# Optimization experiments

Hardware: AMD Instinct MI355X
Metric: run time of the kernel (lower is better)

The kernel has to match this reference:

```python
import jax, jax.numpy as jnp
import numpy as np

V, I, H, OUT = 50000, 512, 1024, 2   # node_size, input_dim, hidden_dim, out_dim
P, L = 256, 64                       # num paths, max path length
NH = 32                              # num attention heads
HD = H // NH


def setup_inputs() -> dict:
    key = jax.random.key(0)
    ks = jax.random.split(key, 10)
    paths = jax.random.randint(ks[0], (P, L), 0, V)          # padded path token ids
    lengths = jax.random.randint(ks[1], (P,), 1, L + 1)       # true path lengths in [1, L]
    g = lambda k, shape, s: jax.random.normal(k, shape, jnp.float32) * s
    return {
        "paths": paths,
        "lengths": lengths,
        "emb_table": g(ks[2], (V, I), 0.1),
        "W_ih": g(ks[3], (4 * H, I), 0.02),
        "W_hh": g(ks[4], (4 * H, H), 0.02),
        "b_ih": jnp.zeros((4 * H,), jnp.float32),
        "b_hh": jnp.zeros((4 * H,), jnp.float32),
        "W_in": g(ks[5], (3 * H, H), 0.02),   # packed q,k,v in_proj (torch layout)
        "b_in": jnp.zeros((3 * H,), jnp.float32),
        "W_out": g(ks[6], (H, H), 0.02),
        "b_out": jnp.zeros((H,), jnp.float32),
        "W_lin": g(ks[7], (OUT, H), 0.02),
        "b_lin": jnp.zeros((OUT,), jnp.float32),
    }


def reference(paths, lengths, emb_table, W_ih, W_hh, b_ih, b_hh,
              W_in, b_in, W_out, b_out, W_lin, b_lin):
    p = paths.shape[0]
    x = emb_table[paths]                 # [P, L, I] (batched embedding of all ragged paths)
    xs = jnp.swapaxes(x, 0, 1)           # [L, P, I] time-major for scan
    b = b_ih + b_hh

    def step(carry, xt):                 # single-layer LSTM, torch gate order i,f,g,o
        h, c = carry
        gates = xt @ W_ih.T + h @ W_hh.T + b          # [P, 4H]
        i_g, f_g, g_g, o_g = jnp.split(gates, 4, axis=-1)
        c = jax.nn.sigmoid(f_g) * c + jax.nn.sigmoid(i_g) * jnp.tanh(g_g)
        h = jax.nn.sigmoid(o_g) * jnp.tanh(c)
        return (h, c), h

    h0 = jnp.zeros((p, H), x.dtype)
    _, hs = jax.lax.scan(step, (h0, h0), xs)          # [L, P, H]
    # final hidden of each path at its true length (equiv. to per-path h_n in the torch loop)
    final_h = hs[lengths - 1, jnp.arange(p)]          # [P, H]
    sum_hidden = final_h[None]                        # [1, P, H]  (seq=1, batch=P)

    # nn.MultiheadAttention(sum_hidden, sum_hidden, sum_hidden), seq_len = 1
    qkv = sum_hidden @ W_in.T + b_in                  # [1, P, 3H]
    q, k, v = jnp.split(qkv, 3, axis=-1)
    qh = q.reshape(1, p, NH, HD)
    kh = k.reshape(1, p, NH, HD)
    vh = v.reshape(1, p, NH, HD)
    scale = 1.0 / np.sqrt(HD).astype(np.float32)
    scores = jnp.einsum('qpnd,kpnd->pnqk', qh * scale, kh)   # [P, NH, 1, 1]
    attn = jax.nn.softmax(scores, axis=-1)
    ctx = jnp.einsum('pnqk,kpnd->qpnd', attn, vh).reshape(1, p, H)
    attn_out = ctx @ W_out.T + b_out                  # [1, P, H]

    # MaxPool2d((P,1)) on (C=1, H=P, W=hidden): max over the P paths
    pooled = jnp.max(attn_out, axis=1, keepdims=True)  # [1, 1, H]
    out = jax.nn.sigmoid(pooled @ W_lin.T + b_lin)     # [1, 1, OUT]
    return out
```

## Files before the change

kernel.cpp:

```cpp
#include <hip/hip_runtime.h>
#include <stdint.h>

typedef unsigned short u16;
typedef unsigned int u32;
typedef __attribute__((ext_vector_type(8))) short s16x8;
typedef __attribute__((ext_vector_type(4))) float f32x4;

#define P_ 256
#define L_ 64
#define IDIM 512
#define H_ 1024

__device__ __forceinline__ u16 f2bf(float f){union{float f;u32 u;}v;v.f=f;u32 u=v.u;return (u16)((u+0x7FFFu+((u>>16)&1u))>>16);}
__device__ __forceinline__ float sigf(float x){return 1.0f/(1.0f+__expf(-x));}
__device__ __forceinline__ float tanhf_(float x){return 1.0f-2.0f/(__expf(2.0f*x)+1.0f);}

__device__ __forceinline__ s16x8 pack8v(float4 a, float4 b){
  s16x8 r;
  r[0]=(short)f2bf(a.x); r[1]=(short)f2bf(a.y); r[2]=(short)f2bf(a.z); r[3]=(short)f2bf(a.w);
  r[4]=(short)f2bf(b.x); r[5]=(short)f2bf(b.y); r[6]=(short)f2bf(b.z); r[7]=(short)f2bf(b.w);
  return r;
}
__device__ __forceinline__ s16x8 pack8(const float* s){
  return pack8v(*(const float4*)s, *(const float4*)(s+4));
}
__device__ __forceinline__ void st16_coh(u16* addr, s16x8 v){
  asm volatile("global_store_dwordx4 %0, %1, off sc0 sc1" :: "v"(addr), "v"(v) : "memory");
}
__device__ __forceinline__ void st_pair(u16* addr, float hv, int lane){
  u32 b = (u32)f2bf(hv);
  u32 other = __shfl_xor(b, 1);
  if ((lane & 1) == 0) {
    u32 w = b | (other << 16);
    __hip_atomic_store((u32*)addr, w, __ATOMIC_RELAXED, __HIP_MEMORY_SCOPE_AGENT);
  }
}
__device__ __forceinline__ void poll_ctr(u32* ctr, u32 target, int wid, int lane){
  if (wid == 0 && lane == 0) {
    while (__hip_atomic_load(ctr, __ATOMIC_RELAXED, __HIP_MEMORY_SCOPE_AGENT) < target)
      __builtin_amdgcn_s_sleep(2);
  }
  asm volatile("" ::: "memory");
  __syncthreads();
}

__global__ void __launch_bounds__(256, 1)
tagger_net(const int* __restrict__ paths, const int* __restrict__ lengths,
           const float* __restrict__ emb,
           const float* __restrict__ Wih, const float* __restrict__ Whh,
           const float* __restrict__ bih, const float* __restrict__ bhh,
           const float* __restrict__ Win, const float* __restrict__ bin,
           const float* __restrict__ Wout, const float* __restrict__ bout,
           const float* __restrict__ Wlin, const float* __restrict__ blin,
           u16* __restrict__ X, u16* __restrict__ Hbuf,
           u16* __restrict__ vbuf, float* __restrict__ pmax,
           u32* ctrs, float* __restrict__ out)
{
  __shared__ __align__(16) float S[16384];
  const int tid  = threadIdx.x;
  const int wid  = tid >> 6, lane = tid & 63;
  const int lrow = lane & 15, lgrp = lane >> 4;
  const int bid  = blockIdx.x;
  const int g = bid >> 6, jb = bid & 63;
  const int p0 = g * 64, j0 = jb * 16;
  u32* ctr = ctrs + g * 64;

  for (int it = 0; it < 16; ++it) {
    int e = (it * 256 + tid) * 8;
    int row = e >> 9, col = e & 511;
    int tok = paths[(p0 + row) * L_ + jb];
    const float* s = emb + (size_t)tok * IDIM + col;
    float4 a = *(const float4*)s, b4 = *(const float4*)(s + 4);
    st16_coh(X + ((size_t)jb * P_ + p0 + row) * IDIM + col, pack8v(a, b4));
  }
#pragma unroll
  for (int i = 0; i < 2; ++i) {
    int idx = tid * 2 + i;
    int row = idx >> 3, cp = idx & 7;
    __hip_atomic_store((u32*)&Hbuf[(size_t)(p0 + row) * H_ + j0 + cp * 2], 0u,
                       __ATOMIC_RELAXED, __HIP_MEMORY_SCOPE_AGENT);
  }
  __syncthreads();
  if (tid == 0) __hip_atomic_fetch_add(ctr, 1u, __ATOMIC_RELAXED, __HIP_MEMORY_SCOPE_AGENT);

  s16x8 breg[12][4];
#pragma unroll
  for (int i = 0; i < 12; ++i) {
    const int k = (wid + 4 * i) * 32 + lgrp * 8;
#pragma unroll
    for (int fn = 0; fn < 4; ++fn) {
      const int n = fn * H_ + j0 + lrow;
      const float* src = (k < IDIM) ? (Wih + (size_t)n * IDIM + k)
                                    : (Whh + (size_t)n * H_ + (k - IDIM));
      breg[i][fn] = pack8(src);
    }
  }

  const int prow = p0 + wid * 16 + lgrp * 4;
  int lenr[4]; float biasv[4];
#pragma unroll
  for (int r2 = 0; r2 < 4; ++r2) lenr[r2] = lengths[prow + r2];
#pragma unroll
  for (int fn = 0; fn < 4; ++fn) {
    int n = fn * H_ + j0 + lrow;
    biasv[fn] = bih[n] + bhh[n];
  }
  float cst[4] = {0.f,0.f,0.f,0.f}, hst[4] = {0.f,0.f,0.f,0.f};

  poll_ctr(ctr, 64u, wid, lane);

  const size_t aX = (size_t)(p0 + lrow) * IDIM + lgrp * 8;
  const size_t aH = (size_t)(p0 + lrow) * H_   + lgrp * 8;

  s16x8 fx[4][4];
#define LOADX(T) do { \
    const u16* Xt_ = X + (size_t)(T) * (P_ * IDIM) + aX; \
    _Pragma("unroll") \
    for (int i_ = 0; i_ < 4; ++i_) { \
      const int k0_ = wid * 32 + i_ * 128; \
      _Pragma("unroll") \
      for (int fm_ = 0; fm_ < 4; ++fm_) \
        fx[i_][fm_] = *(const s16x8*)(Xt_ + (size_t)fm_ * (16 * IDIM) + k0_); \
    } } while (0)

  LOADX(0);

  for (int t = 0; t < L_; ++t) {
    const u16* Hr = Hbuf + (size_t)t * (P_ * H_);
    u16*       Hw = Hbuf + (size_t)(t + 1) * (P_ * H_);

    f32x4 acc[4][4];
#pragma unroll
    for (int a = 0; a < 4; ++a)
#pragma unroll
      for (int b = 0; b < 4; ++b)
#pragma unroll
        for (int e = 0; e < 4; ++e) acc[a][b][e] = 0.0f;

#pragma unroll
    for (int i = 0; i < 4; ++i)
#pragma unroll
      for (int fm = 0; fm < 4; ++fm)
#pragma unroll
        for (int fn = 0; fn < 4; ++fn)
          acc[fm][fn] = __builtin_amdgcn_mfma_f32_16x16x32_bf16(fx[i][fm], breg[i][fn], acc[fm][fn], 0, 0, 0);

    poll_ctr(ctr, 64u * (u32)(t + 1), wid, lane);

    const u16* Hp = Hr + aH;
#pragma unroll
    for (int half = 0; half < 2; ++half) {
      s16x8 fh[4][4];
#pragma unroll
      for (int i = 0; i < 4; ++i) {
        const int kh = wid * 32 + (half * 4 + i) * 128;
#pragma unroll
        for (int fm = 0; fm < 4; ++fm)
          fh[i][fm] = *(const s16x8*)(Hp + (size_t)fm * (16 * H_) + kh);
      }
#pragma unroll
      for (int i = 0; i < 4; ++i)
#pragma unroll
        for (int fm = 0; fm < 4; ++fm)
#pragma unroll
          for (int fn = 0; fn < 4; ++fn)
            acc[fm][fn] = __builtin_amdgcn_mfma_f32_16x16x32_bf16(fh[i][fm], breg[4 + half * 4 + i][fn], acc[fm][fn], 0, 0, 0);
    }

    const int tp1 = (t < L_ - 1) ? (t + 1) : (L_ - 1);
    LOADX(tp1);

#pragma unroll
    for (int fm = 0; fm < 4; ++fm)
#pragma unroll
      for (int fn = 0; fn < 4; ++fn)
        *(f32x4*)&S[((wid * 16) + fm * 4 + fn) * 256 + lane * 4] = acc[fm][fn];
    __syncthreads();
    f32x4 red[4];
#pragma unroll
    for (int fn = 0; fn < 4; ++fn) {
      red[fn] = *(const f32x4*)&S[(wid * 4 + fn) * 256 + lane * 4];
#pragma unroll
      for (int w = 1; w < 4; ++w)
        red[fn] += *(const f32x4*)&S[(w * 16 + wid * 4 + fn) * 256 + lane * 4];
    }

#pragma unroll
    for (int r2 = 0; r2 < 4; ++r2) {
      if (t < lenr[r2]) {
        float gi = red[0][r2] + biasv[0];
        float gf = red[1][r2] + biasv[1];
        float gg = red[2][r2] + biasv[2];
        float go = red[3][r2] + biasv[3];
        float cn = sigf(gf) * cst[r2] + sigf(gi) * tanhf_(gg);
        cst[r2] = cn;
        hst[r2] = sigf(go) * tanhf_(cn);
      }
      st_pair(&Hw[(size_t)(prow + r2) * H_ + j0 + lrow], hst[r2], lane);
    }
    __syncthreads();
    if (tid == 0) __hip_atomic_fetch_add(ctr, 1u, __ATOMIC_RELAXED, __HIP_MEMORY_SCOPE_AGENT);
  }

  const u16* hfin = Hbuf + (size_t)L_ * (P_ * H_);
  poll_ctr(ctr, 64u * 65u, wid, lane);

  {
    f32x4 acc2[4];
#pragma unroll
    for (int a = 0; a < 4; ++a)
#pragma unroll
      for (int e = 0; e < 4; ++e) acc2[a][e] = 0.0f;
    const u16* hp = hfin + aH;
    const float* wv = Win + (size_t)(2 * H_ + j0 + lrow) * H_;
#pragma unroll
    for (int ic = 0; ic < 8; ++ic) {
      const int k0 = wid * 256 + ic * 32;
      s16x8 fbv = pack8(wv + k0 + lgrp * 8);
#pragma unroll
      for (int fm = 0; fm < 4; ++fm) {
        s16x8 fav = *(const s16x8*)(hp + (size_t)fm * (16 * H_) + k0);
        acc2[fm] = __builtin_amdgcn_mfma_f32_16x16x32_bf16(fav, fbv, acc2[fm], 0, 0, 0);
      }
    }
#pragma unroll
    for (int fm = 0; fm < 4; ++fm)
      *(f32x4*)&S[(wid * 4 + fm) * 256 + lane * 4] = acc2[fm];
    __syncthreads();
    f32x4 rv = *(const f32x4*)&S[(wid) * 256 + lane * 4];
#pragma unroll
    for (int w = 1; w < 4; ++w)
      rv += *(const f32x4*)&S[(w * 4 + wid) * 256 + lane * 4];
    float bvj = bin[2 * H_ + j0 + lrow];
#pragma unroll
    for (int r2 = 0; r2 < 4; ++r2)
      st_pair(&vbuf[(size_t)(prow + r2) * H_ + j0 + lrow], rv[r2] + bvj, lane);
  }
  __syncthreads();
  if (tid == 0) __hip_atomic_fetch_add(ctr, 1u, __ATOMIC_RELAXED, __HIP_MEMORY_SCOPE_AGENT);
  poll_ctr(ctr, 64u * 66u, wid, lane);

  {
    f32x4 acc2[4];
#pragma unroll
    for (int a = 0; a < 4; ++a)
#pragma unroll
      for (int e = 0; e < 4; ++e) acc2[a][e] = 0.0f;
    const u16* vp = vbuf + aH;
    const float* wo = Wout + (size_t)(j0 + lrow) * H_;
#pragma unroll
    for (int ic = 0; ic < 8; ++ic) {
      const int k0 = wid * 256 + ic * 32;
      s16x8 fbv = pack8(wo + k0 + lgrp * 8);
#pragma unroll
      for (int fm = 0; fm < 4; ++fm) {
        s16x8 fav = *(const s16x8*)(vp + (size_t)fm * (16 * H_) + k0);
        acc2[fm] = __builtin_amdgcn_mfma_f32_16x16x32_bf16(fav, fbv, acc2[fm], 0, 0, 0);
      }
    }
#pragma unroll
    for (int fm = 0; fm < 4; ++fm)
      *(f32x4*)&S[(wid * 4 + fm) * 256 + lane * 4] = acc2[fm];
    __syncthreads();
    f32x4 rv = *(const f32x4*)&S[(wid) * 256 + lane * 4];
#pragma unroll
    for (int w = 1; w < 4; ++w)
      rv += *(const f32x4*)&S[(w * 4 + wid) * 256 + lane * 4];
    float bo = bout[j0 + lrow];
    float m = fmaxf(fmaxf(rv[0], rv[1]), fmaxf(rv[2], rv[3])) + bo;
    __syncthreads();
    S[(wid * 4 + lgrp) * 16 + lrow] = m;
    __syncthreads();
    if (tid < 16) {
      float mx = S[tid];
#pragma unroll
      for (int s2 = 1; s2 < 16; ++s2) mx = fmaxf(mx, S[s2 * 16 + tid]);
      __hip_atomic_store(&pmax[(size_t)g * H_ + j0 + tid], mx, __ATOMIC_RELAXED, __HIP_MEMORY_SCOPE_AGENT);
    }
  }
  __syncthreads();
  if (tid == 0) __hip_atomic_fetch_add(ctr, 1u, __ATOMIC_RELAXED, __HIP_MEMORY_SCOPE_AGENT);

  if (bid != 0) return;

  if (wid == 0 && lane == 0) {
    for (int g2 = 0; g2 < 4; ++g2)
      while (__hip_atomic_load(ctrs + g2 * 64, __ATOMIC_RELAXED, __HIP_MEMORY_SCOPE_AGENT) < 64u * 67u)
        __builtin_amdgcn_s_sleep(2);
  }
  asm volatile("" ::: "memory");
  __syncthreads();
  {
    int j4 = tid * 4;
    float s0 = 0.f, s1 = 0.f;
#pragma unroll
    for (int e = 0; e < 4; ++e) {
      float pv = pmax[j4 + e];
#pragma unroll
      for (int gg2 = 1; gg2 < 4; ++gg2) pv = fmaxf(pv, pmax[gg2 * H_ + j4 + e]);
      s0 += pv * Wlin[j4 + e];
      s1 += pv * Wlin[H_ + j4 + e];
    }
    S[tid] = s0; S[256 + tid] = s1;
    __syncthreads();
    for (int s2 = 128; s2 > 0; s2 >>= 1) {
      if (tid < s2) { S[tid] += S[tid + s2]; S[256 + tid] += S[256 + tid + s2]; }
      __syncthreads();
    }
    if (tid == 0) {
      out[0] = sigf(S[0] + blin[0]);
      out[1] = sigf(S[256] + blin[1]);
    }
  }
}

extern "C" void kernel_launch(void* const* d_in, const int* in_sizes, int n_in,
                              void* d_out, int out_size, void* d_ws, size_t ws_size,
                              hipStream_t stream) {
  const int*   paths   = (const int*)d_in[0];
  const int*   lengths = (const int*)d_in[1];
  const float* emb     = (const float*)d_in[2];
  const float* Wih     = (const float*)d_in[3];
  const float* Whh     = (const float*)d_in[4];
  const float* bih     = (const float*)d_in[5];
  const float* bhh     = (const float*)d_in[6];
  const float* Win     = (const float*)d_in[7];
  const float* bin     = (const float*)d_in[8];
  const float* Wout    = (const float*)d_in[9];
  const float* bout    = (const float*)d_in[10];
  const float* Wlin    = (const float*)d_in[11];
  const float* blin    = (const float*)d_in[12];
  float* out = (float*)d_out;

  char* ws = (char*)d_ws;
  u32*   ctrs   = (u32*)  (ws);
  float* pmax   = (float*)(ws + 4096);
  u16*   X      = (u16*)  (ws + 32768);
  u16*   Hbuf   = (u16*)  (ws + 16810240);
  u16*   vbuf   = (u16*)  (ws + 50888960);

  hipMemsetAsync(ctrs, 0, 1024, stream);
  tagger_net<<<256, 256, 0, stream>>>(paths, lengths, emb, Wih, Whh, bih, bhh,
                                      Win, bin, Wout, bout, Wlin, blin,
                                      X, Hbuf, vbuf, pmax, ctrs, out);
}
```

Before: 630.7 us.

## Split LSTM hidden columns across twice as many persistent blocks with just-in-time embedding gather

Doubles the grid from 256 to 512 blocks. Each block now owns 8 hidden units instead of 16, packing all four gates into two 16-wide MFMA N-tiles, and gates are recombined with a lane shuffle. The upfront embedding gather for all timesteps is replaced by gathering step t+2 inside the recurrence, and H loads are interleaved with MFMAs in smaller chunks. This halves per-block weight registers and per-step MFMA work to shorten the serial step latency. In exchange it doubles the blocks participating in each per-group counter barrier, and it requires two blocks per CU to be co-resident or the spin barrier deadlocks.

```diff
diff --git a/kernel.cpp b/kernel.cpp
--- a/kernel.cpp
+++ b/kernel.cpp
@@ -10,6 +10,7 @@
 #define L_ 64
 #define IDIM 512
 #define H_ 1024
+#define PH (P_ * H_)
 
 __device__ __forceinline__ u16 f2bf(float f){union{float f;u32 u;}v;v.f=f;u32 u=v.u;return (u16)((u+0x7FFFu+((u>>16)&1u))>>16);}
 __device__ __forceinline__ float sigf(float x){return 1.0f/(1.0f+__expf(-x));}
@@ -27,24 +28,16 @@
 __device__ __forceinline__ void st16_coh(u16* addr, s16x8 v){
   asm volatile("global_store_dwordx4 %0, %1, off sc0 sc1" :: "v"(addr), "v"(v) : "memory");
 }
-__device__ __forceinline__ void st_pair(u16* addr, float hv, int lane){
-  u32 b = (u32)f2bf(hv);
-  u32 other = __shfl_xor(b, 1);
-  if ((lane & 1) == 0) {
-    u32 w = b | (other << 16);
-    __hip_atomic_store((u32*)addr, w, __ATOMIC_RELAXED, __HIP_MEMORY_SCOPE_AGENT);
-  }
-}
 __device__ __forceinline__ void poll_ctr(u32* ctr, u32 target, int wid, int lane){
   if (wid == 0 && lane == 0) {
     while (__hip_atomic_load(ctr, __ATOMIC_RELAXED, __HIP_MEMORY_SCOPE_AGENT) < target)
-      __builtin_amdgcn_s_sleep(2);
+      __builtin_amdgcn_s_sleep(1);
   }
   asm volatile("" ::: "memory");
   __syncthreads();
 }
 
-__global__ void __launch_bounds__(256, 1)
+__global__ void __launch_bounds__(256, 2)
 tagger_net(const int* __restrict__ paths, const int* __restrict__ lengths,
            const float* __restrict__ emb,
            const float* __restrict__ Wih, const float* __restrict__ Whh,
@@ -56,40 +49,37 @@
            u16* __restrict__ vbuf, float* __restrict__ pmax,
            u32* ctrs, float* __restrict__ out)
 {
-  __shared__ __align__(16) float S[16384];
+  __shared__ __align__(16) float S[8192];
   const int tid  = threadIdx.x;
   const int wid  = tid >> 6, lane = tid & 63;
   const int lrow = lane & 15, lgrp = lane >> 4;
   const int bid  = blockIdx.x;
-  const int g = bid >> 6, jb = bid & 63;
-  const int p0 = g * 64, j0 = jb * 16;
+  const int g = bid >> 7, jb2 = bid & 127;
+  const int p0 = g * 64, j0 = jb2 * 8;
   u32* ctr = ctrs + g * 64;
 
-  for (int it = 0; it < 16; ++it) {
-    int e = (it * 256 + tid) * 8;
-    int row = e >> 9, col = e & 511;
-    int tok = paths[(p0 + row) * L_ + jb];
-    const float* s = emb + (size_t)tok * IDIM + col;
-    float4 a = *(const float4*)s, b4 = *(const float4*)(s + 4);
-    st16_coh(X + ((size_t)jb * P_ + p0 + row) * IDIM + col, pack8v(a, b4));
-  }
-#pragma unroll
-  for (int i = 0; i < 2; ++i) {
-    int idx = tid * 2 + i;
-    int row = idx >> 3, cp = idx & 7;
-    __hip_atomic_store((u32*)&Hbuf[(size_t)(p0 + row) * H_ + j0 + cp * 2], 0u,
+  if (wid == 0) {
+    int t0 = jb2 >> 6, row = jb2 & 63;
+    int tok = paths[(p0 + row) * L_ + t0];
+    const float* s = emb + (size_t)tok * IDIM + lane * 8;
+    st16_coh(X + ((size_t)t0 * P_ + p0 + row) * IDIM + lane * 8,
+             pack8v(*(const float4*)s, *(const float4*)(s + 4)));
+  }
+  {
+    int row = tid >> 2, cp = (tid & 3) * 2;
+    __hip_atomic_store((u32*)&Hbuf[(size_t)(p0 + row) * H_ + j0 + cp], 0u,
                        __ATOMIC_RELAXED, __HIP_MEMORY_SCOPE_AGENT);
   }
   __syncthreads();
   if (tid == 0) __hip_atomic_fetch_add(ctr, 1u, __ATOMIC_RELAXED, __HIP_MEMORY_SCOPE_AGENT);
 
-  s16x8 breg[12][4];
+  s16x8 breg[12][2];
 #pragma unroll
   for (int i = 0; i < 12; ++i) {
     const int k = (wid + 4 * i) * 32 + lgrp * 8;
 #pragma unroll
-    for (int fn = 0; fn < 4; ++fn) {
-      const int n = fn * H_ + j0 + lrow;
+    for (int fn = 0; fn < 2; ++fn) {
+      const int n = (fn * 2 + (lrow >> 3)) * H_ + j0 + (lrow & 7);
       const float* src = (k < IDIM) ? (Wih + (size_t)n * IDIM + k)
                                     : (Whh + (size_t)n * H_ + (k - IDIM));
       breg[i][fn] = pack8(src);
@@ -97,185 +87,204 @@
   }
 
   const int prow = p0 + wid * 16 + lgrp * 4;
-  int lenr[4]; float biasv[4];
-#pragma unroll
-  for (int r2 = 0; r2 < 4; ++r2) lenr[r2] = lengths[prow + r2];
-#pragma unroll
-  for (int fn = 0; fn < 4; ++fn) {
-    int n = fn * H_ + j0 + lrow;
-    biasv[fn] = bih[n] + bhh[n];
-  }
+  int lenr[4];
+#pragma unroll
+  for (int r = 0; r < 4; ++r) lenr[r] = lengths[prow + r];
+  const int ju = j0 + (lrow & 7);
+  const float bias_i = bih[ju] + bhh[ju];
+  const float bias_f = bih[H_ + ju] + bhh[H_ + ju];
+  const float bias_g = bih[2 * H_ + ju] + bhh[2 * H_ + ju];
+  const float bias_o = bih[3 * H_ + ju] + bhh[3 * H_ + ju];
   float cst[4] = {0.f,0.f,0.f,0.f}, hst[4] = {0.f,0.f,0.f,0.f};
-
-  poll_ctr(ctr, 64u, wid, lane);
 
   const size_t aX = (size_t)(p0 + lrow) * IDIM + lgrp * 8;
   const size_t aH = (size_t)(p0 + lrow) * H_   + lgrp * 8;
 
-  s16x8 fx[4][4];
-#define LOADX(T) do { \
+  poll_ctr(ctr, 128u, wid, lane);
+
+#define MM(FR, I0) do { \
+    _Pragma("unroll") \
+    for (int j_ = 0; j_ < 2; ++j_) \
+      _Pragma("unroll") \
+      for (int fm_ = 0; fm_ < 4; ++fm_) \
+        _Pragma("unroll") \
+        for (int fn_ = 0; fn_ < 2; ++fn_) \
+          acc[fm_][fn_] = __builtin_amdgcn_mfma_f32_16x16x32_bf16(FR[j_][fm_], breg[(I0)+j_][fn_], acc[fm_][fn_], 0, 0, 0); \
+  } while (0)
+
+#define LDX2(DST, T, C0) do { \
     const u16* Xt_ = X + (size_t)(T) * (P_ * IDIM) + aX; \
     _Pragma("unroll") \
-    for (int i_ = 0; i_ < 4; ++i_) { \
-      const int k0_ = wid * 32 + i_ * 128; \
+    for (int j_ = 0; j_ < 2; ++j_) { \
+      const int k0_ = (wid + 4 * ((C0) + j_)) * 32; \
       _Pragma("unroll") \
       for (int fm_ = 0; fm_ < 4; ++fm_) \
-        fx[i_][fm_] = *(const s16x8*)(Xt_ + (size_t)fm_ * (16 * IDIM) + k0_); \
+        DST[j_][fm_] = *(const s16x8*)(Xt_ + (size_t)fm_ * (16 * IDIM) + k0_); \
     } } while (0)
 
-  LOADX(0);
+#define LDH2(DST, C0) do { \
+    _Pragma("unroll") \
+    for (int j_ = 0; j_ < 2; ++j_) { \
+      const int kh_ = wid * 32 + ((C0) + j_) * 128; \
+      _Pragma("unroll") \
+      for (int fm_ = 0; fm_ < 4; ++fm_) \
+        DST[j_][fm_] = *(const s16x8*)(Hp + (size_t)fm_ * (16 * H_) + kh_); \
+    } } while (0)
+
+  s16x8 fx[2][4];
+  LDX2(fx, 0, 0);
 
   for (int t = 0; t < L_; ++t) {
-    const u16* Hr = Hbuf + (size_t)t * (P_ * H_);
-    u16*       Hw = Hbuf + (size_t)(t + 1) * (P_ * H_);
-
-    f32x4 acc[4][4];
+    u16* Hw = Hbuf + (size_t)(t + 1) * PH;
+
+    if (wid == 0 && jb2 < 64 && t + 2 < L_) {
+      int tok = paths[(p0 + jb2) * L_ + (t + 2)];
+      const float* s = emb + (size_t)tok * IDIM + lane * 8;
+      st16_coh(X + ((size_t)(t + 2) * P_ + p0 + jb2) * IDIM + lane * 8,
+               pack8v(*(const float4*)s, *(const float4*)(s + 4)));
+    }
+    s16x8 fx2[2][4];
+    LDX2(fx2, t, 2);
+
+    poll_ctr(ctr, 128u * (u32)(t + 1), wid, lane);
+
+    f32x4 acc[4][2];
 #pragma unroll
     for (int a = 0; a < 4; ++a)
 #pragma unroll
-      for (int b = 0; b < 4; ++b)
+      for (int b = 0; b < 2; ++b)
 #pragma unroll
         for (int e = 0; e < 4; ++e) acc[a][b][e] = 0.0f;
 
-#pragma unroll
-    for (int i = 0; i < 4; ++i)
-#pragma unroll
-      for (int fm = 0; fm < 4; ++fm)
-#pragma unroll
-        for (int fn = 0; fn < 4; ++fn)
-          acc[fm][fn] = __builtin_amdgcn_mfma_f32_16x16x32_bf16(fx[i][fm], breg[i][fn], acc[fm][fn], 0, 0, 0);
-
-    poll_ctr(ctr, 64u * (u32)(t + 1), wid, lane);
-
-    const u16* Hp = Hr + aH;
-#pragma unroll
-    for (int half = 0; half < 2; ++half) {
-      s16x8 fh[4][4];
-#pragma unroll
-      for (int i = 0; i < 4; ++i) {
-        const int kh = wid * 32 + (half * 4 + i) * 128;
-#pragma unroll
-        for (int fm = 0; fm < 4; ++fm)
-          fh[i][fm] = *(const s16x8*)(Hp + (size_t)fm * (16 * H_) + kh);
+    const u16* Hp = Hbuf + (size_t)t * PH + aH;
+    s16x8 fhA[2][4], fhB[2][4], fhC[2][4], fhD[2][4];
+    LDH2(fhA, 0); LDH2(fhB, 2);
+    MM(fx, 0);
+    MM(fx2, 2);
+    MM(fhA, 4);  LDH2(fhC, 4);
+    MM(fhB, 6);  LDH2(fhD, 6);
+    MM(fhC, 8);
+    { const int tn = (t + 1 < L_) ? t + 1 : t; LDX2(fx, tn, 0); }
+    MM(fhD, 10);
+
+#pragma unroll
+    for (int fm = 0; fm < 4; ++fm)
+#pragma unroll
+      for (int fn = 0; fn < 2; ++fn)
+        *(f32x4*)&S[((wid * 8) + fm * 2 + fn) * 256 + lane * 4] = acc[fm][fn];
+    __syncthreads();
+    f32x4 red[2];
+#pragma unroll
+    for (int fn = 0; fn < 2; ++fn) {
+      red[fn] = *(const f32x4*)&S[(wid * 2 + fn) * 256 + lane * 4];
+#pragma unroll
+      for (int w = 1; w < 4; ++w)
+        red[fn] += *(const f32x4*)&S[(w * 8 + wid * 2 + fn) * 256 + lane * 4];
+    }
+
+    const bool low = (lrow < 8);
+#pragma unroll
+    for (int r = 0; r < 4; ++r) {
+      float o0 = __shfl_xor(red[0][r], 8);
+      float o1 = __shfl_xor(red[1][r], 8);
+      float gi = (low ? red[0][r] : o0) + bias_i;
+      float gf = (low ? o0 : red[0][r]) + bias_f;
+      float gg = (low ? red[1][r] : o1) + bias_g;
+      float go = (low ? o1 : red[1][r]) + bias_o;
+      if (t < lenr[r]) {
+        float cn = sigf(gf) * cst[r] + sigf(gi) * tanhf_(gg);
+        cst[r] = cn;
+        hst[r] = sigf(go) * tanhf_(cn);
       }
-#pragma unroll
-      for (int i = 0; i < 4; ++i)
-#pragma unroll
-        for (int fm = 0; fm < 4; ++fm)
-#pragma unroll
-          for (int fn = 0; fn < 4; ++fn)
-            acc[fm][fn] = __builtin_amdgcn_mfma_f32_16x16x32_bf16(fh[i][fm], breg[4 + half * 4 + i][fn], acc[fm][fn], 0, 0, 0);
-    }
-
-    const int tp1 = (t < L_ - 1) ? (t + 1) : (L_ - 1);
-    LOADX(tp1);
-
-#pragma unroll
-    for (int fm = 0; fm < 4; ++fm)
-#pragma unroll
-      for (int fn = 0; fn < 4; ++fn)
-        *(f32x4*)&S[((wid * 16) + fm * 4 + fn) * 256 + lane * 4] = acc[fm][fn];
-    __syncthreads();
-    f32x4 red[4];
-#pragma unroll
-    for (int fn = 0; fn < 4; ++fn) {
-      red[fn] = *(const f32x4*)&S[(wid * 4 + fn) * 256 + lane * 4];
-#pragma unroll
-      for (int w = 1; w < 4; ++w)
-        red[fn] += *(const f32x4*)&S[(w * 16 + wid * 4 + fn) * 256 + lane * 4];
-    }
-
-#pragma unroll
-    for (int r2 = 0; r2 < 4; ++r2) {
-      if (t < lenr[r2]) {
-        float gi = red[0][r2] + biasv[0];
-        float gf = red[1][r2] + biasv[1];
-        float gg = red[2][r2] + biasv[2];
-        float go = red[3][r2] + biasv[3];
-        float cn = sigf(gf) * cst[r2] + sigf(gi) * tanhf_(gg);
-        cst[r2] = cn;
-        hst[r2] = sigf(go) * tanhf_(cn);
-      }
-      st_pair(&Hw[(size_t)(prow + r2) * H_ + j0 + lrow], hst[r2], lane);
+      u32 b = (u32)f2bf(hst[r]);
+      u32 oth = __shfl_xor(b, 1);
+      if (low && (lane & 1) == 0)
+        __hip_atomic_store((u32*)&Hw[(size_t)(prow + r) * H_ + j0 + lrow], b | (oth << 16),
+                           __ATOMIC_RELAXED, __HIP_MEMORY_SCOPE_AGENT);
     }
     __syncthreads();
     if (tid == 0) __hip_atomic_fetch_add(ctr, 1u, __ATOMIC_RELAXED, __HIP_MEMORY_SCOPE_AGENT);
   }
 
-  const u16* hfin = Hbuf + (size_t)L_ * (P_ * H_);
-  poll_ctr(ctr, 64u * 65u, wid, lane);
+  poll_ctr(ctr, 128u * 65u, wid, lane);
+  const u16* hfin = Hbuf + (size_t)L_ * PH;
 
   {
-    f32x4 acc2[4];
+    f32x4 a2[4];
 #pragma unroll
     for (int a = 0; a < 4; ++a)
 #pragma unroll
-      for (int e = 0; e < 4; ++e) acc2[a][e] = 0.0f;
+      for (int e = 0; e < 4; ++e) a2[a][e] = 0.0f;
     const u16* hp = hfin + aH;
-    const float* wv = Win + (size_t)(2 * H_ + j0 + lrow) * H_;
+    const float* wv = Win + (size_t)(2 * H_ + ju) * H_;
 #pragma unroll
     for (int ic = 0; ic < 8; ++ic) {
       const int k0 = wid * 256 + ic * 32;
-      s16x8 fbv = pack8(wv + k0 + lgrp * 8);
+      s16x8 fb = pack8(wv + k0 + lgrp * 8);
 #pragma unroll
       for (int fm = 0; fm < 4; ++fm) {
-        s16x8 fav = *(const s16x8*)(hp + (size_t)fm * (16 * H_) + k0);
-        acc2[fm] = __builtin_amdgcn_mfma_f32_16x16x32_bf16(fav, fbv, acc2[fm], 0, 0, 0);
+        s16x8 fa = *(const s16x8*)(hp + (size_t)fm * (16 * H_) + k0);
+        a2[fm] = __builtin_amdgcn_mfma_f32_16x16x32_bf16(fa, fb, a2[fm], 0, 0, 0);
       }
     }
 #pragma unroll
     for (int fm = 0; fm < 4; ++fm)
-      *(f32x4*)&S[(wid * 4 + fm) * 256 + lane * 4] = acc2[fm];
+      *(f32x4*)&S[(wid * 4 + fm) * 256 + lane * 4] = a2[fm];
     __syncthreads();
     f32x4 rv = *(const f32x4*)&S[(wid) * 256 + lane * 4];
 #pragma unroll
     for (int w = 1; w < 4; ++w)
       rv += *(const f32x4*)&S[(w * 4 + wid) * 256 + lane * 4];
-    float bvj = bin[2 * H_ + j0 + lrow];
-#pragma unroll
-    for (int r2 = 0; r2 < 4; ++r2)
-      st_pair(&vbuf[(size_t)(prow + r2) * H_ + j0 + lrow], rv[r2] + bvj, lane);
+    const float bvj = bin[2 * H_ + ju];
+#pragma unroll
+    for (int r = 0; r < 4; ++r) {
+      u32 b = (u32)f2bf(rv[r] + bvj);
+      u32 oth = __shfl_xor(b, 1);
+      if (lrow < 8 && (lane & 1) == 0)
+        __hip_atomic_store((u32*)&vbuf[(size_t)(prow + r) * H_ + j0 + lrow], b | (oth << 16),
+                           __ATOMIC_RELAXED, __HIP_MEMORY_SCOPE_AGENT);
+    }
   }
   __syncthreads();
   if (tid == 0) __hip_atomic_fetch_add(ctr, 1u, __ATOMIC_RELAXED, __HIP_MEMORY_SCOPE_AGENT);
-  poll_ctr(ctr, 64u * 66u, wid, lane);
+  poll_ctr(ctr, 128u * 66u, wid, lane);
 
   {
-    f32x4 acc2[4];
+    f32x4 a2[4];
 #pragma unroll
     for (int a = 0; a < 4; ++a)
 #pragma unroll
-      for (int e = 0; e < 4; ++e) acc2[a][e] = 0.0f;
+      for (int e = 0; e < 4; ++e) a2[a][e] = 0.0f;
     const u16* vp = vbuf + aH;
-    const float* wo = Wout + (size_t)(j0 + lrow) * H_;
+    const float* wo = Wout + (size_t)ju * H_;
 #pragma unroll
     for (int ic = 0; ic < 8; ++ic) {
       const int k0 = wid * 256 + ic * 32;
-      s16x8 fbv = pack8(wo + k0 + lgrp * 8);
+      s16x8 fb = pack8(wo + k0 + lgrp * 8);
 #pragma unroll
       for (int fm = 0; fm < 4; ++fm) {
-        s16x8 fav = *(const s16x8*)(vp + (size_t)fm * (16 * H_) + k0);
-        acc2[fm] = __builtin_amdgcn_mfma_f32_16x16x32_bf16(fav, fbv, acc2[fm], 0, 0, 0);
+        s16x8 fa = *(const s16x8*)(vp + (size_t)fm * (16 * H_) + k0);
+        a2[fm] = __builtin_amdgcn_mfma_f32_16x16x32_bf16(fa, fb, a2[fm], 0, 0, 0);
       }
     }
 #pragma unroll
     for (int fm = 0; fm < 4; ++fm)
-      *(f32x4*)&S[(wid * 4 + fm) * 256 + lane * 4] = acc2[fm];
+      *(f32x4*)&S[(wid * 4 + fm) * 256 + lane * 4] = a2[fm];
     __syncthreads();
     f32x4 rv = *(const f32x4*)&S[(wid) * 256 + lane * 4];
 #pragma unroll
     for (int w = 1; w < 4; ++w)
       rv += *(const f32x4*)&S[(w * 4 + wid) * 256 + lane * 4];
-    float bo = bout[j0 + lrow];
-    float m = fmaxf(fmaxf(rv[0], rv[1]), fmaxf(rv[2], rv[3])) + bo;
-    __syncthreads();
-    S[(wid * 4 + lgrp) * 16 + lrow] = m;
-    __syncthreads();
-    if (tid < 16) {
+    float m = fmaxf(fmaxf(rv[0], rv[1]), fmaxf(rv[2], rv[3])) + bout[ju];
+    __syncthreads();
+    S[(wid * 4 + lgrp) * 8 + (lrow & 7)] = m;
+    __syncthreads();
+    if (tid < 8) {
       float mx = S[tid];
 #pragma unroll
-      for (int s2 = 1; s2 < 16; ++s2) mx = fmaxf(mx, S[s2 * 16 + tid]);
-      __hip_atomic_store(&pmax[(size_t)g * H_ + j0 + tid], mx, __ATOMIC_RELAXED, __HIP_MEMORY_SCOPE_AGENT);
+      for (int s2 = 1; s2 < 16; ++s2) mx = fmaxf(mx, S[s2 * 8 + tid]);
+      __hip_atomic_store(&pmax[(size_t)g * H_ + j0 + tid], mx,
+                         __ATOMIC_RELAXED, __HIP_MEMORY_SCOPE_AGENT);
     }
   }
   __syncthreads();
@@ -285,8 +294,8 @@
 
   if (wid == 0 && lane == 0) {
     for (int g2 = 0; g2 < 4; ++g2)
-      while (__hip_atomic_load(ctrs + g2 * 64, __ATOMIC_RELAXED, __HIP_MEMORY_SCOPE_AGENT) < 64u * 67u)
-        __builtin_amdgcn_s_sleep(2);
+      while (__hip_atomic_load(ctrs + g2 * 64, __ATOMIC_RELAXED, __HIP_MEMORY_SCOPE_AGENT) < 128u * 67u)
+        __builtin_amdgcn_s_sleep(1);
   }
   asm volatile("" ::: "memory");
   __syncthreads();
@@ -340,7 +349,7 @@
   u16*   vbuf   = (u16*)  (ws + 50888960);
 
   hipMemsetAsync(ctrs, 0, 1024, stream);
-  tagger_net<<<256, 256, 0, stream>>>(paths, lengths, emb, Wih, Whh, bih, bhh,
+  tagger_net<<<512, 256, 0, stream>>>(paths, lengths, emb, Wih, Whh, bih, bhh,
                                       Win, bin, Wout, bout, Wlin, blin,
                                       X, Hbuf, vbuf, pmax, ctrs, out);
 }
```

Result: slower. 1.072 ms (+69.9%).
